# Kernel tuning notes

Measured on AMD Instinct MI355X. Metric: run time of the kernel, lower is better.

## Reference

```python
import jax, jax.numpy as jnp
import numpy as np

N = 100000   # nodes
E = 1600000  # edges (avg degree 16)
D = 64       # in_dim
H = 64       # hidden_dim
NEG_SLOPE = 0.2


def setup_inputs() -> dict:
    key = jax.random.key(0)
    ks = jax.random.split(key, 10)
    s = 0.1  # param init scale
    return {
        "x": jax.random.normal(ks[0], (N, D), jnp.float32),
        "edge_index": jax.random.randint(ks[1], (2, E), 0, N, dtype=jnp.int64),
        "h": jax.random.normal(ks[2], (1, N, H), jnp.float32),
        "c": jax.random.normal(ks[3], (1, N, H), jnp.float32),
        "W_gat": jax.random.normal(ks[4], (D, H), jnp.float32) * s,
        "att_src": jax.random.normal(ks[5], (H,), jnp.float32) * s,
        "att_dst": jax.random.normal(ks[6], (H,), jnp.float32) * s,
        "bias_gat": jax.random.normal(ks[7], (H,), jnp.float32) * s,
        "W_ih": jax.random.normal(ks[8], (4 * H, H), jnp.float32) * s,
        "W_hh": jax.random.normal(ks[9], (4 * H, H), jnp.float32) * s,
    }


def reference(x, edge_index, h, c, W_gat, att_src, att_dst, bias_gat, W_ih, W_hh):
    src, dst = edge_index[0], edge_index[1]  # message j -> i

    # ---- Breadth: GATConv (heads=1) + tanh ----
    xs = x @ W_gat                             # [N, H] projected features
    a_src = xs @ att_src                       # [N]
    a_dst = xs @ att_dst                       # [N]
    e = jax.nn.leaky_relu(a_src[src] + a_dst[dst], NEG_SLOPE)  # [E]
    # scatter-softmax over incoming edges of each destination node
    m = jax.lax.stop_gradient(jax.ops.segment_max(e, dst, num_segments=N))
    p = jnp.exp(e - m[dst])
    z = jax.ops.segment_sum(p, dst, num_segments=N)
    alpha = p / (z[dst] + 1e-16)               # [E]
    agg = jax.ops.segment_sum(xs[src] * alpha[:, None], dst, num_segments=N)
    xb = jnp.tanh(agg + bias_gat)              # [N, H]

    # ---- Depth: single-step bias-free LSTM ----
    h0, c0 = h[0], c[0]                        # [N, H]
    gates = xb @ W_ih.T + h0 @ W_hh.T          # [N, 4H]
    i, f, g, o = jnp.split(gates, 4, axis=-1)  # torch gate order i,f,g,o
    c1 = jax.nn.sigmoid(f) * c0 + jax.nn.sigmoid(i) * jnp.tanh(g)
    h1 = jax.nn.sigmoid(o) * jnp.tanh(c1)
    return h1, h1[None], c1[None]
```

## Files before the change

kernel.cpp:

```cpp
#include <hip/hip_runtime.h>
#include <cmath>

#define NN 100000
#define EE 1600000
#define NB 1563
#define CAP 1344
#define EPB 25
#define NTILE 6250
#define PROJB 1563
#define CVTB 3125

using bf16x8 = __attribute__((ext_vector_type(8))) __bf16;
using f32x4  = __attribute__((ext_vector_type(4))) float;

__device__ __forceinline__ unsigned short f2bf(float f) {
  __bf16 b = (__bf16)f;
  return __builtin_bit_cast(unsigned short, b);
}
__device__ __forceinline__ float bflo(unsigned int u) {
  return __uint_as_float(u << 16);
}
__device__ __forceinline__ float bfhi(unsigned int u) {
  return __uint_as_float(u & 0xffff0000u);
}
__device__ __forceinline__ float sigmoidf_(float v) {
  return 1.0f / (1.0f + __expf(-v));
}
__device__ __forceinline__ float tanhfast(float v) {
  return 1.0f - 2.0f / (1.0f + __expf(2.0f * v));
}
__device__ __forceinline__ bf16x8 cvt8(float4 a, float4 b) {
  bf16x8 r;
  r[0]=(__bf16)a.x; r[1]=(__bf16)a.y; r[2]=(__bf16)a.z; r[3]=(__bf16)a.w;
  r[4]=(__bf16)b.x; r[5]=(__bf16)b.y; r[6]=(__bf16)b.z; r[7]=(__bf16)b.w;
  return r;
}

__global__ __launch_bounds__(128) void k_prep(
    const float* __restrict__ Wih, const float* __restrict__ Whh,
    const float* __restrict__ Wg,
    unsigned short* __restrict__ wperm, unsigned short* __restrict__ wgp)
{
  if (blockIdx.x < 256) {
    const int p = blockIdx.x, k = threadIdx.x;
    const int g = p & 3;
    const int h = (p >> 4) + ((p >> 2) & 3) * 16;
    const int row = g*64 + h;
    const float v = (k < 64) ? Wih[row*64 + k] : Whh[row*64 + (k - 64)];
    const int gp = (k >> 3) ^ (p & 15);
    wperm[p*128 + gp*8 + (k & 7)] = f2bf(v);
  } else {
    for (int idx = threadIdx.x; idx < 4096; idx += 128) {
      const int lane = idx >> 6, r = idx & 63;
      const int nt = r >> 4, kf = (r >> 3) & 1, j = r & 7;
      const int m = lane & 15, quad = lane >> 4;
      wgp[idx] = f2bf(Wg[(kf*32 + quad*8 + j)*64 + nt*16 + m]);
    }
  }
}

__global__ __launch_bounds__(256) void k_binproj(
    const int* __restrict__ ei, int* __restrict__ bcursor,
    unsigned int* __restrict__ binned,
    const float* __restrict__ x, const unsigned short* __restrict__ wgp,
    const float* __restrict__ att_s, const float* __restrict__ att_d,
    unsigned short* __restrict__ xs16, float* __restrict__ a_src,
    float* __restrict__ a_dst,
    const float* __restrict__ h0, unsigned short* __restrict__ h16)
{
  if (blockIdx.x < 256) {
    __shared__ int cnt[NB];
    __shared__ int gbase[NB];
    const int tid = threadIdx.x;
    const size_t base = (size_t)blockIdx.x * 256 * EPB;

    for (int b = tid; b < NB; b += 256) cnt[b] = 0;
    __syncthreads();

    unsigned int pay[EPB];
    int bidx[EPB], pos[EPB];
    #pragma unroll
    for (int j = 0; j < EPB; ++j) {
      const size_t e = base + (size_t)j*256 + tid;
      if (e < EE) {
        const int s = ei[e];
        const int d = ei[EE + e];
        bidx[j] = d >> 6;
        pay[j] = (unsigned)s | ((unsigned)(d & 63) << 17);
        pos[j] = atomicAdd(&cnt[bidx[j]], 1);
      } else {
        bidx[j] = -1;
      }
    }
    __syncthreads();

    for (int b = tid; b < NB; b += 256) {
      const int c = cnt[b];
      gbase[b] = c ? atomicAdd(&bcursor[b*16], c) : 0;
    }
    __syncthreads();

    #pragma unroll
    for (int j = 0; j < EPB; ++j) {
      if (bidx[j] >= 0) {
        const int g = gbase[bidx[j]] + pos[j];
        if (g < CAP) binned[(size_t)bidx[j]*CAP + g] = pay[j];
      }
    }
  } else if (blockIdx.x < 256 + PROJB) {
    const int lane = threadIdx.x & 63;
    const int wave = threadIdx.x >> 6;
    const int tile = (blockIdx.x - 256) * 4 + wave;
    if (tile >= NTILE) return;
    const int m = lane & 15, quad = lane >> 4;

    bf16x8 bfrag[4][2];
    {
      const unsigned short* wp = wgp + lane*64;
      #pragma unroll
      for (int nt = 0; nt < 4; ++nt)
        #pragma unroll
        for (int kf = 0; kf < 2; ++kf)
          bfrag[nt][kf] = *(const bf16x8*)(wp + nt*16 + kf*8);
    }

    const int row = tile*16 + m;
    bf16x8 afrag[2];
    #pragma unroll
    for (int kf = 0; kf < 2; ++kf) {
      const float4* p = (const float4*)(x + (size_t)row*64 + kf*32 + quad*8);
      afrag[kf] = cvt8(p[0], p[1]);
    }

    f32x4 acc[4];
    #pragma unroll
    for (int nt = 0; nt < 4; ++nt) acc[nt] = f32x4{0.f, 0.f, 0.f, 0.f};
    #pragma unroll
    for (int nt = 0; nt < 4; ++nt)
      #pragma unroll
      for (int kf = 0; kf < 2; ++kf)
        acc[nt] = __builtin_amdgcn_mfma_f32_16x16x32_bf16(
            afrag[kf], bfrag[nt][kf], acc[nt], 0, 0, 0);

    float ss[4] = {0.f,0.f,0.f,0.f}, sd[4] = {0.f,0.f,0.f,0.f};
    #pragma unroll
    for (int nt = 0; nt < 4; ++nt) {
      const float av = att_s[nt*16 + m], dv = att_d[nt*16 + m];
      #pragma unroll
      for (int r = 0; r < 4; ++r) {
        const float v = acc[nt][r];
        xs16[(size_t)(tile*16 + quad*4 + r)*64 + nt*16 + m] = f2bf(v);
        ss[r] += v * av;
        sd[r] += v * dv;
      }
    }
    #pragma unroll
    for (int off = 1; off < 16; off <<= 1) {
      #pragma unroll
      for (int r = 0; r < 4; ++r) {
        ss[r] += __shfl_xor(ss[r], off);
        sd[r] += __shfl_xor(sd[r], off);
      }
    }
    if (m == 0) {
      #pragma unroll
      for (int r = 0; r < 4; ++r) {
        a_src[tile*16 + quad*4 + r] = ss[r];
        a_dst[tile*16 + quad*4 + r] = sd[r];
      }
    }
  } else {
    const int idx = (blockIdx.x - 256 - PROJB)*256 + threadIdx.x;
    const float* p = h0 + (size_t)idx*8;
    const bf16x8 v = cvt8(*(const float4*)p, *(const float4*)(p + 4));
    *(bf16x8*)(h16 + (size_t)idx*8) = v;
  }
}

__global__ __launch_bounds__(256) void k_agg(
    const int* __restrict__ bcursor, const unsigned int* __restrict__ binned,
    const float* __restrict__ a_src, const float* __restrict__ a_dst,
    const unsigned short* __restrict__ xs16, const float* __restrict__ bias,
    unsigned short* __restrict__ xb16)
{
  __shared__ uint2 csre[CAP + 8];
  __shared__ float zsum[64], invzsh[64], adsh[64];
  __shared__ int cnt[64], offs[64], cursor[64];
  const int b = blockIdx.x;
  const int tid = threadIdx.x;
  const int ne = min(bcursor[b*16], CAP);

  if (tid < 64) {
    cnt[tid] = 0;
    zsum[tid] = 0.f;
    const int node = b*64 + tid;
    adsh[tid] = (node < NN) ? a_dst[node] : 0.f;
  }
  __syncthreads();

  unsigned int w6[6];
  float pv6[6];
  {
    float as6[6];
    #pragma unroll
    for (int k = 0; k < 6; ++k) {
      const int i = tid + k*256;
      w6[k] = (i < ne) ? binned[(size_t)b*CAP + i] : 0u;
    }
    #pragma unroll
    for (int k = 0; k < 6; ++k) {
      const int i = tid + k*256;
      as6[k] = (i < ne) ? a_src[w6[k] & 0x1FFFFu] : 0.f;
    }
    #pragma unroll
    for (int k = 0; k < 6; ++k) {
      const int i = tid + k*256;
      if (i < ne) {
        const int dl = (int)((w6[k] >> 17) & 63u);
        float ev = as6[k] + adsh[dl];
        ev = (ev >= 0.f) ? ev : 0.2f*ev;
        const float pv = __expf(ev);
        pv6[k] = pv;
        atomicAdd(&cnt[dl], 1);
        atomicAdd(&zsum[dl], pv);
      }
    }
  }
  __syncthreads();

  if (tid < 64) {
    const int v = cnt[tid];
    int inc = v;
    #pragma unroll
    for (int dd = 1; dd < 64; dd <<= 1) {
      const int o = __shfl_up(inc, dd, 64);
      if (tid >= dd) inc += o;
    }
    offs[tid] = inc - v;
    cursor[tid] = inc - v;
    invzsh[tid] = 1.f / (zsum[tid] + 1e-16f);
  }
  __syncthreads();

  #pragma unroll
  for (int k = 0; k < 6; ++k) {
    const int i = tid + k*256;
    if (i < ne) {
      const unsigned int w = w6[k];
      const int dl = (int)((w >> 17) & 63u);
      const int pos = atomicAdd(&cursor[dl], 1);
      csre[pos] = make_uint2(w & 0x1FFFFu, __float_as_uint(pv6[k]));
    }
  }
  __syncthreads();

  const int lane = tid & 63;
  const int wv = tid >> 6;
  const int grp = lane >> 4, l16 = lane & 15;
  const float4 b4 = *(const float4*)(bias + l16*4);
  const unsigned short* xrow = xs16 + l16*4;
  for (int t = 0; t < 16; ++t) {
    const int nl = wv*16 + t;
    const int node = b*64 + nl;
    if (node >= NN) break;
    const int bse = offs[nl];
    const int dg = cnt[nl];
    float acc0=0.f, acc1=0.f, acc2=0.f, acc3=0.f;
    uint2 sp = csre[bse + grp];
    for (int e = grp; e < dg; e += 4) {
      const uint2 spn = csre[bse + e + 4];
      const float pv = __uint_as_float(sp.y);
      const uint2 rw = *(const uint2*)(xrow + (size_t)sp.x*64);
      acc0 += pv*bflo(rw.x); acc1 += pv*bfhi(rw.x);
      acc2 += pv*bflo(rw.y); acc3 += pv*bfhi(rw.y);
      sp = spn;
    }
    #pragma unroll
    for (int off = 16; off < 64; off <<= 1) {
      acc0 += __shfl_xor(acc0, off);
      acc1 += __shfl_xor(acc1, off);
      acc2 += __shfl_xor(acc2, off);
      acc3 += __shfl_xor(acc3, off);
    }
    if (lane < 16) {
      const float invz = invzsh[nl];
      ushort4 o;
      o.x = f2bf(tanhfast(acc0*invz + b4.x));
      o.y = f2bf(tanhfast(acc1*invz + b4.y));
      o.z = f2bf(tanhfast(acc2*invz + b4.z));
      o.w = f2bf(tanhfast(acc3*invz + b4.w));
      *(ushort4*)(xb16 + (size_t)node*64 + l16*4) = o;
    }
  }
}

__global__ __launch_bounds__(1024, 2) void k_lstm(
    const unsigned short* __restrict__ xb16, const unsigned short* __restrict__ h16,
    const float* __restrict__ c0, const unsigned short* __restrict__ wperm,
    float* __restrict__ out)
{
  __shared__ unsigned short wlds[256*128];
  const int tid = threadIdx.x;
  {
    const float4* gs = (const float4*)wperm;
    float4* ls = (float4*)wlds;
    #pragma unroll
    for (int i = 0; i < 4; ++i) ls[tid + i*1024] = gs[tid + i*1024];
  }
  __syncthreads();

  const int w = tid >> 6, lane = tid & 63;
  const int wv = w & 3, tsub = w >> 2;
  const int m = lane & 15, quad = lane >> 4;

  const int q32 = (m >> 2) & 3;
  const int base = (wv*64 + m)*256 + ((quad ^ (m & 3)) << 4);
  const char* lb = (const char*)wlds;
  const int a0 = base + ((0 ^ q32) << 6);
  const int a1 = base + ((1 ^ q32) << 6);
  const int a2 = base + ((2 ^ q32) << 6);
  const int a3 = base + ((3 ^ q32) << 6);

  for (int tg = blockIdx.x; tg < PROJB; tg += gridDim.x) {
    const int tile = tg*4 + tsub;
    if (tile >= NTILE) continue;
    const int node = tile*16 + m;

    bf16x8 bfr[4];
    bfr[0] = *(const bf16x8*)(xb16 + (size_t)node*64 + quad*8);
    bfr[1] = *(const bf16x8*)(xb16 + (size_t)node*64 + 32 + quad*8);
    bfr[2] = *(const bf16x8*)(h16 + (size_t)node*64 + quad*8);
    bfr[3] = *(const bf16x8*)(h16 + (size_t)node*64 + 32 + quad*8);

    f32x4 acc[4];
    #pragma unroll
    for (int u = 0; u < 4; ++u) acc[u] = f32x4{0.f, 0.f, 0.f, 0.f};
    #pragma unroll
    for (int u = 0; u < 4; ++u) {
      const int uo = u*4096;
      const bf16x8 w0 = *(const bf16x8*)(lb + a0 + uo);
      const bf16x8 w1 = *(const bf16x8*)(lb + a1 + uo);
      const bf16x8 w2 = *(const bf16x8*)(lb + a2 + uo);
      const bf16x8 w3 = *(const bf16x8*)(lb + a3 + uo);
      acc[u] = __builtin_amdgcn_mfma_f32_16x16x32_bf16(w0, bfr[0], acc[u], 0, 0, 0);
      acc[u] = __builtin_amdgcn_mfma_f32_16x16x32_bf16(w1, bfr[1], acc[u], 0, 0, 0);
      acc[u] = __builtin_amdgcn_mfma_f32_16x16x32_bf16(w2, bfr[2], acc[u], 0, 0, 0);
      acc[u] = __builtin_amdgcn_mfma_f32_16x16x32_bf16(w3, bfr[3], acc[u], 0, 0, 0);
    }

    const size_t obase = (size_t)node*64 + quad*16 + wv*4;
    const float4 cv = *(const float4*)(c0 + obase);
    const float cvv[4] = {cv.x, cv.y, cv.z, cv.w};
    float h1a[4], c1a[4];
    #pragma unroll
    for (int u = 0; u < 4; ++u) {
      const float gi = acc[u][0], gf = acc[u][1];
      const float gg = acc[u][2], go = acc[u][3];
      const float c1 = sigmoidf_(gf)*cvv[u] + sigmoidf_(gi)*tanhfast(gg);
      h1a[u] = sigmoidf_(go)*tanhfast(c1);
      c1a[u] = c1;
    }
    const float4 hv  = make_float4(h1a[0], h1a[1], h1a[2], h1a[3]);
    const float4 c1v = make_float4(c1a[0], c1a[1], c1a[2], c1a[3]);
    *(float4*)(out + obase) = hv;
    *(float4*)(out + (size_t)NN*64 + obase) = hv;
    *(float4*)(out + (size_t)2*NN*64 + obase) = c1v;
  }
}

extern "C" void kernel_launch(void* const* d_in, const int* in_sizes, int n_in,
                              void* d_out, int out_size, void* d_ws, size_t ws_size,
                              hipStream_t stream) {
  const float* x    = (const float*)d_in[0];
  const int*   ei   = (const int*)d_in[1];
  const float* h    = (const float*)d_in[2];
  const float* c    = (const float*)d_in[3];
  const float* Wg   = (const float*)d_in[4];
  const float* atts = (const float*)d_in[5];
  const float* attd = (const float*)d_in[6];
  const float* bg   = (const float*)d_in[7];
  const float* Wih  = (const float*)d_in[8];
  const float* Whh  = (const float*)d_in[9];
  float* out = (float*)d_out;

  char* w = (char*)d_ws;
  unsigned short* xs16  = (unsigned short*)w; w += (size_t)NN*64*2;
  unsigned short* xb16  = (unsigned short*)w; w += (size_t)NN*64*2;
  unsigned short* h16   = (unsigned short*)w; w += (size_t)NN*64*2;
  unsigned short* wperm = (unsigned short*)w; w += (size_t)256*128*2;
  unsigned short* wgp   = (unsigned short*)w; w += (size_t)4096*2;
  unsigned int*   binned= (unsigned int*)w;  w += (size_t)NB*CAP*4;
  float* a_src = (float*)w; w += (size_t)NN*4;
  float* a_dst = (float*)w; w += (size_t)NN*4;
  int* bcursor = (int*)w;   w += (size_t)NB*16*4;

  hipMemsetAsync(bcursor, 0, (size_t)NB*16*4, stream);

  k_prep    <<<257, 128, 0, stream>>>(Wih, Whh, Wg, wperm, wgp);
  k_binproj <<<256 + PROJB + CVTB, 256, 0, stream>>>(
      ei, bcursor, binned, x, wgp, atts, attd, xs16, a_src, a_dst, h, h16);
  k_agg     <<<NB, 256, 0, stream>>>(bcursor, binned, a_src, a_dst, xs16, bg, xb16);
  k_lstm    <<<512, 1024, 0, stream>>>(xb16, h16, c, wperm, out);
}
```

Before: 293.8 us.

## Fold memset into prep, convert h in LSTM, record per-dst slot at count

Removes the hipMemsetAsync by zeroing the bin cursors in extra k_prep blocks. Drops the separate h0-to-bf16 conversion blocks and their workspace buffer; k_lstm now reads fp32 h0 and converts it inline. In k_agg, the per-destination slot is captured from the counting atomic and packed into a staging LDS array, so the second atomic pass and its cursor array go away. The cost is an extra LDS buffer, and the software prefetch of the next edge record in the gather loop is removed.

```diff
diff --git a/kernel.cpp b/kernel.cpp
--- a/kernel.cpp
+++ b/kernel.cpp
@@ -8,7 +8,6 @@
 #define EPB 25
 #define NTILE 6250
 #define PROJB 1563
-#define CVTB 3125
 
 using bf16x8 = __attribute__((ext_vector_type(8))) __bf16;
 using f32x4  = __attribute__((ext_vector_type(4))) float;
@@ -39,7 +38,8 @@
 __global__ __launch_bounds__(128) void k_prep(
     const float* __restrict__ Wih, const float* __restrict__ Whh,
     const float* __restrict__ Wg,
-    unsigned short* __restrict__ wperm, unsigned short* __restrict__ wgp)
+    unsigned short* __restrict__ wperm, unsigned short* __restrict__ wgp,
+    int* __restrict__ bcursor)
 {
   if (blockIdx.x < 256) {
     const int p = blockIdx.x, k = threadIdx.x;
@@ -49,13 +49,17 @@
     const float v = (k < 64) ? Wih[row*64 + k] : Whh[row*64 + (k - 64)];
     const int gp = (k >> 3) ^ (p & 15);
     wperm[p*128 + gp*8 + (k & 7)] = f2bf(v);
-  } else {
+  } else if (blockIdx.x == 256) {
     for (int idx = threadIdx.x; idx < 4096; idx += 128) {
       const int lane = idx >> 6, r = idx & 63;
       const int nt = r >> 4, kf = (r >> 3) & 1, j = r & 7;
       const int m = lane & 15, quad = lane >> 4;
       wgp[idx] = f2bf(Wg[(kf*32 + quad*8 + j)*64 + nt*16 + m]);
     }
+  } else {
+    for (int idx = (blockIdx.x - 257)*128 + threadIdx.x; idx < NB*16;
+         idx += 100*128)
+      bcursor[idx] = 0;
   }
 }
 
@@ -65,8 +69,7 @@
     const float* __restrict__ x, const unsigned short* __restrict__ wgp,
     const float* __restrict__ att_s, const float* __restrict__ att_d,
     unsigned short* __restrict__ xs16, float* __restrict__ a_src,
-    float* __restrict__ a_dst,
-    const float* __restrict__ h0, unsigned short* __restrict__ h16)
+    float* __restrict__ a_dst)
 {
   if (blockIdx.x < 256) {
     __shared__ int cnt[NB];
@@ -107,7 +110,7 @@
         if (g < CAP) binned[(size_t)bidx[j]*CAP + g] = pay[j];
       }
     }
-  } else if (blockIdx.x < 256 + PROJB) {
+  } else {
     const int lane = threadIdx.x & 63;
     const int wave = threadIdx.x >> 6;
     const int tile = (blockIdx.x - 256) * 4 + wave;
@@ -169,11 +172,6 @@
         a_dst[tile*16 + quad*4 + r] = sd[r];
       }
     }
-  } else {
-    const int idx = (blockIdx.x - 256 - PROJB)*256 + threadIdx.x;
-    const float* p = h0 + (size_t)idx*8;
-    const bf16x8 v = cvt8(*(const float4*)p, *(const float4*)(p + 4));
-    *(bf16x8*)(h16 + (size_t)idx*8) = v;
   }
 }
 
@@ -183,9 +181,10 @@
     const unsigned short* __restrict__ xs16, const float* __restrict__ bias,
     unsigned short* __restrict__ xb16)
 {
-  __shared__ uint2 csre[CAP + 8];
+  __shared__ uint2 raw2[CAP];
+  __shared__ uint2 csre[CAP];
   __shared__ float zsum[64], invzsh[64], adsh[64];
-  __shared__ int cnt[64], offs[64], cursor[64];
+  __shared__ int cnt[64], offs[64];
   const int b = blockIdx.x;
   const int tid = threadIdx.x;
   const int ne = min(bcursor[b*16], CAP);
@@ -198,9 +197,8 @@
   }
   __syncthreads();
 
-  unsigned int w6[6];
-  float pv6[6];
   {
+    unsigned int w6[6];
     float as6[6];
     #pragma unroll
     for (int k = 0; k < 6; ++k) {
@@ -220,9 +218,10 @@
         float ev = as6[k] + adsh[dl];
         ev = (ev >= 0.f) ? ev : 0.2f*ev;
         const float pv = __expf(ev);
-        pv6[k] = pv;
-        atomicAdd(&cnt[dl], 1);
+        const int pos = atomicAdd(&cnt[dl], 1);
         atomicAdd(&zsum[dl], pv);
+        raw2[i] = make_uint2((w6[k] & 0x7FFFFFu) | ((unsigned)pos << 23),
+                             __float_as_uint(pv));
       }
     }
   }
@@ -237,7 +236,6 @@
       if (tid >= dd) inc += o;
     }
     offs[tid] = inc - v;
-    cursor[tid] = inc - v;
     invzsh[tid] = 1.f / (zsum[tid] + 1e-16f);
   }
   __syncthreads();
@@ -246,10 +244,10 @@
   for (int k = 0; k < 6; ++k) {
     const int i = tid + k*256;
     if (i < ne) {
-      const unsigned int w = w6[k];
-      const int dl = (int)((w >> 17) & 63u);
-      const int pos = atomicAdd(&cursor[dl], 1);
-      csre[pos] = make_uint2(w & 0x1FFFFu, __float_as_uint(pv6[k]));
+      const uint2 r = raw2[i];
+      const int dl = (int)((r.x >> 17) & 63u);
+      const int pos = (int)(r.x >> 23);
+      csre[offs[dl] + pos] = make_uint2(r.x & 0x1FFFFu, r.y);
     }
   }
   __syncthreads();
@@ -266,14 +264,12 @@
     const int bse = offs[nl];
     const int dg = cnt[nl];
     float acc0=0.f, acc1=0.f, acc2=0.f, acc3=0.f;
-    uint2 sp = csre[bse + grp];
     for (int e = grp; e < dg; e += 4) {
-      const uint2 spn = csre[bse + e + 4];
+      const uint2 sp = csre[bse + e];
       const float pv = __uint_as_float(sp.y);
       const uint2 rw = *(const uint2*)(xrow + (size_t)sp.x*64);
       acc0 += pv*bflo(rw.x); acc1 += pv*bfhi(rw.x);
       acc2 += pv*bflo(rw.y); acc3 += pv*bfhi(rw.y);
-      sp = spn;
     }
     #pragma unroll
     for (int off = 16; off < 64; off <<= 1) {
@@ -295,7 +291,7 @@
 }
 
 __global__ __launch_bounds__(1024, 2) void k_lstm(
-    const unsigned short* __restrict__ xb16, const unsigned short* __restrict__ h16,
+    const unsigned short* __restrict__ xb16, const float* __restrict__ h0,
     const float* __restrict__ c0, const unsigned short* __restrict__ wperm,
     float* __restrict__ out)
 {
@@ -329,8 +325,12 @@
     bf16x8 bfr[4];
     bfr[0] = *(const bf16x8*)(xb16 + (size_t)node*64 + quad*8);
     bfr[1] = *(const bf16x8*)(xb16 + (size_t)node*64 + 32 + quad*8);
-    bfr[2] = *(const bf16x8*)(h16 + (size_t)node*64 + quad*8);
-    bfr[3] = *(const bf16x8*)(h16 + (size_t)node*64 + 32 + quad*8);
+    {
+      const float* p0 = h0 + (size_t)node*64 + quad*8;
+      bfr[2] = cvt8(*(const float4*)p0, *(const float4*)(p0 + 4));
+      const float* p1 = h0 + (size_t)node*64 + 32 + quad*8;
+      bfr[3] = cvt8(*(const float4*)p1, *(const float4*)(p1 + 4));
+    }
 
     f32x4 acc[4];
     #pragma unroll
@@ -386,7 +386,6 @@
   char* w = (char*)d_ws;
   unsigned short* xs16  = (unsigned short*)w; w += (size_t)NN*64*2;
   unsigned short* xb16  = (unsigned short*)w; w += (size_t)NN*64*2;
-  unsigned short* h16   = (unsigned short*)w; w += (size_t)NN*64*2;
   unsigned short* wperm = (unsigned short*)w; w += (size_t)256*128*2;
   unsigned short* wgp   = (unsigned short*)w; w += (size_t)4096*2;
   unsigned int*   binned= (unsigned int*)w;  w += (size_t)NB*CAP*4;
@@ -394,11 +393,9 @@
   float* a_dst = (float*)w; w += (size_t)NN*4;
   int* bcursor = (int*)w;   w += (size_t)NB*16*4;
 
-  hipMemsetAsync(bcursor, 0, (size_t)NB*16*4, stream);
-
-  k_prep    <<<257, 128, 0, stream>>>(Wih, Whh, Wg, wperm, wgp);
-  k_binproj <<<256 + PROJB + CVTB, 256, 0, stream>>>(
-      ei, bcursor, binned, x, wgp, atts, attd, xs16, a_src, a_dst, h, h16);
+  k_prep    <<<357, 128, 0, stream>>>(Wih, Whh, Wg, wperm, wgp, bcursor);
+  k_binproj <<<256 + PROJB, 256, 0, stream>>>(
+      ei, bcursor, binned, x, wgp, atts, attd, xs16, a_src, a_dst);
   k_agg     <<<NB, 256, 0, stream>>>(bcursor, binned, a_src, a_dst, xs16, bg, xb16);
-  k_lstm    <<<512, 1024, 0, stream>>>(xb16, h16, c, wperm, out);
-}
+  k_lstm    <<<512, 1024, 0, stream>>>(xb16, h, c, wperm, out);
+}
```

Measured after the change: 298.7 us. Within noise of the previous version (+1.7%).
